# Performance work log

Measured on AMD Instinct MI355X. Metric: run time of the kernel, lower is better.

Reference implementation:

```python
import jax, jax.numpy as jnp
import numpy as np

SEQ_LEN = 2048
EMBED = 1024
HIDDEN = 1024
BATCH = 4


def setup_inputs() -> dict:
    key = jax.random.key(0)
    ks = jax.random.split(key, 7)
    # xavier_uniform for weights: limit = sqrt(6/(fan_in+fan_out))
    lim = float(np.sqrt(6.0 / (EMBED + HIDDEN)))
    blim = float(1.0 / np.sqrt(EMBED))  # torch Linear default bias init U(-1/sqrt(fan_in), ...)
    inputs = jax.random.normal(ks[0], (BATCH, SEQ_LEN, EMBED), dtype=jnp.float32)
    Wq = jax.random.uniform(ks[1], (HIDDEN, EMBED), jnp.float32, -lim, lim)
    Wk = jax.random.uniform(ks[2], (HIDDEN, EMBED), jnp.float32, -lim, lim)
    Wv = jax.random.uniform(ks[3], (HIDDEN, EMBED), jnp.float32, -lim, lim)
    bq = jax.random.uniform(ks[4], (HIDDEN,), jnp.float32, -blim, blim)
    bk = jax.random.uniform(ks[5], (HIDDEN,), jnp.float32, -blim, blim)
    bv = jax.random.uniform(ks[6], (HIDDEN,), jnp.float32, -blim, blim)
    return {"inputs": inputs, "Wq": Wq, "bq": bq, "Wk": Wk, "bk": bk, "Wv": Wv, "bv": bv}


def reference(inputs, Wq, bq, Wk, bk, Wv, bv):
    B, S, E = inputs.shape
    q = jnp.einsum('bse,he->bsh', inputs, Wq) + bq  # [B,S,H]
    k = jnp.einsum('bse,he->bsh', inputs, Wk) + bk
    v = jnp.einsum('bse,he->bsh', inputs, Wv) + bv
    # NOTE: source scales by 1/sqrt(embed_size), not hidden_size
    scores = jnp.einsum('bqh,bkh->bqk', q, k) / jnp.sqrt(jnp.float32(E))
    causal = jnp.tril(jnp.ones((S, S), dtype=bool))  # [S,S]
    scores = jnp.where(causal[None, :, :], scores, -jnp.inf)
    attn = jax.nn.softmax(scores, axis=-1)
    return jnp.einsum('bqk,bkh->bqh', attn, v)
```

## Files before the change

### kernel.cpp

```cpp
#include <hip/hip_runtime.h>
#include <cstdint>
#include <cstddef>
#include <math.h>

typedef unsigned short u16;

#define S_LEN 2048
#define EMB   1024
#define HID   1024
#define NB    4

using bf16x8 = __attribute__((ext_vector_type(8))) __bf16;
using f32x4  = __attribute__((ext_vector_type(4))) float;


__device__ __forceinline__ u16 f2bf(float f) {
  union { float f; uint32_t u; } c; c.f = f;
  uint32_t u = c.u;
  uint32_t r = (u + 0x7fffu + ((u >> 16) & 1u)) >> 16;
  return (u16)r;
}

__device__ __forceinline__ void gld_lds16(const u16* g, u16* l) {
  auto gp = (const __attribute__((address_space(1))) uint32_t*)(uintptr_t)(const void*)g;
  auto lp = (__attribute__((address_space(3))) uint32_t*)(uintptr_t)(void*)l;
  __builtin_amdgcn_global_load_lds(gp, lp, 16, 0, 0);
}


__global__ void cvt_f32_bf16(const float* __restrict__ in, u16* __restrict__ out, int n4) {
  int i = blockIdx.x * blockDim.x + threadIdx.x;
  int stride = gridDim.x * blockDim.x;
  for (; i < n4; i += stride) {
    float4 v = reinterpret_cast<const float4*>(in)[i];
    reinterpret_cast<ushort4*>(out)[i] =
      make_ushort4(f2bf(v.x), f2bf(v.y), f2bf(v.z), f2bf(v.w));
  }
}

__global__ void cvt3_f32_bf16(const float* __restrict__ a, const float* __restrict__ b,
                              const float* __restrict__ c, u16* __restrict__ out, int n4) {
  const float* src = (blockIdx.y == 0) ? a : (blockIdx.y == 1) ? b : c;
  u16* dst = out + (size_t)blockIdx.y * (size_t)n4 * 4;
  int i = blockIdx.x * blockDim.x + threadIdx.x;
  int stride = gridDim.x * blockDim.x;
  for (; i < n4; i += stride) {
    float4 v = reinterpret_cast<const float4*>(src)[i];
    reinterpret_cast<ushort4*>(dst)[i] =
      make_ushort4(f2bf(v.x), f2bf(v.y), f2bf(v.z), f2bf(v.w));
  }
}


template<int EPI>
__global__ __launch_bounds__(512, 2)
void gemm4p(const u16* __restrict__ A, const u16* __restrict__ Bw, void* __restrict__ Cv,
            const float* __restrict__ b0, const float* __restrict__ b1,
            const float* __restrict__ b2, u16* __restrict__ VT,
            int N, int K, long sA, long sB, long sC, float scale)
{
  const int z = blockIdx.z;
  A  += (long)z * sA;
  Bw += (long)z * sB;

  __shared__ __align__(16) u16 smem[49152];

  const int tid = threadIdx.x;
  const int l   = tid & 63;
  const int w   = tid >> 6;
  const int wr  = w >> 2;
  const int wc  = w & 3;

  const int nwg = gridDim.x * gridDim.y;
  const int lin = blockIdx.y * gridDim.x + blockIdx.x;
  const int sw  = (lin & 7) * (nwg >> 3) + (lin >> 3);
  const int bm  = (sw / gridDim.x) * 128;
  const int bn  = (sw % gridDim.x) * 256;

  int kend = K;
  if constexpr (EPI == 3) kend = bm + 128;
  const int NTILE = kend >> 6;

  const int arow = w * 16 + (l >> 2);
  const int acs  = (l & 3) ^ (((l >> 5) & 1) << 1);
  const u16* gbA  = A  + (long)(bm + arow) * K + acs * 8;
  const u16* gbB  = Bw + (long)(bn + arow) * K + acs * 8;
  const u16* gbB2 = gbB + 128L * K;

#define STGH(t, s, dbase)                                                       \
  do {                                                                          \
    const long _o = (long)(t) * 64 + (s) * 32;                                  \
    gld_lds16(gbA  + _o, smem + (dbase) + (s) * 4096 + w * 512);                \
    gld_lds16(gbB  + _o, smem + (dbase) + 8192 + (s) * 8192 + w * 512);         \
    gld_lds16(gbB2 + _o, smem + (dbase) + 8192 + (s) * 8192 + 4096 + w * 512);  \
  } while (0)

  const int lr  = l & 15;
  const int kg  = l >> 4;
  const int kgp = kg ^ (((lr >> 3) & 1) << 1);
  int aoff[4], boff[4];
#pragma unroll
  for (int m = 0; m < 4; ++m) aoff[m] = (wr * 64 + m * 16 + lr) * 32 + kgp * 8;
#pragma unroll
  for (int n = 0; n < 4; ++n) boff[n] = (wc * 64 + n * 16 + lr) * 32 + kgp * 8;

  f32x4 acc[4][4] = {};

  STGH(0, 0, 0);
  STGH(0, 1, 0);
  asm volatile("s_waitcnt vmcnt(0)" ::: "memory");
  __builtin_amdgcn_s_barrier();
  asm volatile("" ::: "memory");

#define PHASE(d, s, STGSTMT)                                                    \
  do {                                                                          \
    const u16* hA = smem + (d) * 24576 + (s) * 4096;                            \
    const u16* hB = smem + (d) * 24576 + 8192 + (s) * 8192;                     \
    bf16x8 av[4], bv[4];                                                        \
    _Pragma("unroll")                                                           \
    for (int m_ = 0; m_ < 4; ++m_)                                              \
      av[m_] = *reinterpret_cast<const bf16x8*>(hA + aoff[m_]);                 \
    _Pragma("unroll")                                                           \
    for (int n_ = 0; n_ < 4; ++n_)                                              \
      bv[n_] = *reinterpret_cast<const bf16x8*>(hB + boff[n_]);                 \
    STGSTMT;                                                                    \
    asm volatile("s_waitcnt vmcnt(3)" ::: "memory");                            \
    __builtin_amdgcn_s_barrier();                                               \
    asm volatile("" ::: "memory");                                              \
    __builtin_amdgcn_s_setprio(1);                                              \
    _Pragma("unroll")                                                           \
    for (int m_ = 0; m_ < 4; ++m_)                                              \
      _Pragma("unroll")                                                         \
      for (int n_ = 0; n_ < 4; ++n_)                                            \
        acc[m_][n_] = __builtin_amdgcn_mfma_f32_16x16x32_bf16(                  \
            av[m_], bv[n_], acc[m_][n_], 0, 0, 0);                              \
    __builtin_amdgcn_s_setprio(0);                                              \
    asm volatile("" ::: "memory");                                              \
  } while (0)

#pragma unroll 1
  for (int i = 0; i < NTILE / 2; ++i) {
    const int t1 = 2 * i + 1;
    const int t2 = (2 * i + 2 < NTILE) ? 2 * i + 2 : NTILE - 1;
    PHASE(0, 0, STGH(t1, 0, 24576));
    PHASE(0, 1, STGH(t1, 1, 24576));
    PHASE(1, 0, STGH(t2, 0, 0));
    PHASE(1, 1, STGH(t2, 1, 0));
  }
#undef PHASE
#undef STGH

  if constexpr (EPI == 3) {
    float* C = (float*)Cv + (long)z * sC;
#pragma unroll
    for (int n = 0; n < 4; ++n) {
      const int col = bn + wc * 64 + n * 16 + lr;
#pragma unroll
      for (int m = 0; m < 4; ++m) {
        const int row0 = bm + wr * 64 + m * 16 + kg * 4;
#pragma unroll
        for (int q = 0; q < 4; ++q)
          C[(long)(row0 + q) * N + col] = acc[m][n][q];
      }
    }
  } else {
    constexpr long M = (long)NB * S_LEN;
    const int sel = bn >> 10;
    const float* bias = (sel == 0) ? b0 : (sel == 1) ? b1 : b2;
    u16* QK = (u16*)Cv;
#pragma unroll
    for (int n = 0; n < 4; ++n) {
      const int col = bn + wc * 64 + n * 16 + lr;
      const int h   = col & (HID - 1);
      const float bbv = bias[h];
#pragma unroll
      for (int m = 0; m < 4; ++m) {
        const int row0 = bm + wr * 64 + m * 16 + kg * 4;
        if (sel < 2) {
          u16* dst = QK + (long)sel * M * HID + (long)row0 * HID + h;
#pragma unroll
          for (int q = 0; q < 4; ++q)
            dst[(long)q * HID] = f2bf(acc[m][n][q] + bbv);
        } else {
          const int b = row0 >> 11;
          const int s = row0 & (S_LEN - 1);
          ushort4 o = make_ushort4(f2bf(acc[m][n][0] + bbv), f2bf(acc[m][n][1] + bbv),
                                   f2bf(acc[m][n][2] + bbv), f2bf(acc[m][n][3] + bbv));
          *reinterpret_cast<ushort4*>(VT + ((long)b * HID + h) * S_LEN + s) = o;
        }
      }
    }
  }
}


__global__ __launch_bounds__(512, 2)
void gemm_pv(const u16* __restrict__ Pm, const u16* __restrict__ VTm, float* __restrict__ Cm)
{
  const int z = blockIdx.z;
  const u16* A = Pm  + (long)z * S_LEN * S_LEN;
  const u16* B = VTm + (long)z * HID * S_LEN;
  float*    Cz = Cm  + (long)z * S_LEN * HID;

  __shared__ __align__(16) u16 smem[32768];

  const int tid = threadIdx.x;
  const int l   = tid & 63;
  const int w   = tid >> 6;
  const int wr  = w >> 2;
  const int wc  = w & 3;
  const int bn  = blockIdx.x * 128;
  const int pr  = blockIdx.y;

  const int lr  = l & 15;
  const int kg  = l >> 4;
  const int kgp = kg ^ (((lr >> 3) & 1) << 1);
  int aoff[4], boff[2];
#pragma unroll
  for (int m = 0; m < 4; ++m) aoff[m] = (wr * 64 + m * 16 + lr) * 32 + kgp * 8;
#pragma unroll
  for (int n = 0; n < 2; ++n) boff[n] = (wc * 32 + n * 16 + lr) * 32 + kgp * 8;

  const int arow = w * 16 + (l >> 2);
  const int acs  = (l & 3) ^ (((l >> 5) & 1) << 1);

#pragma unroll 1
  for (int it = 0; it < 2; ++it) {
    const int bi = (it == 0) ? (15 - pr) : pr;
    const int bm = bi * 128;
    const int NTILE = (bi + 1) * 2;

    const u16* gbA = A + (long)(bm + arow) * S_LEN + acs * 8;
    const u16* gbB = B + (long)(bn + arow) * S_LEN + acs * 8;

#define STGH(t, s, dbase)                                                       \
  do {                                                                          \
    const long _o = (long)(t) * 64 + (s) * 32;                                  \
    gld_lds16(gbA + _o, smem + (dbase) + (s) * 4096 + w * 512);                 \
    gld_lds16(gbB + _o, smem + (dbase) + 8192 + (s) * 4096 + w * 512);          \
  } while (0)

    if (it) {
      __builtin_amdgcn_s_barrier();
      asm volatile("" ::: "memory");
    }

    f32x4 acc[4][2] = {};

    STGH(0, 0, 0);
    STGH(0, 1, 0);
    asm volatile("s_waitcnt vmcnt(0)" ::: "memory");
    __builtin_amdgcn_s_barrier();
    asm volatile("" ::: "memory");

#define PHASE(d, s, STGSTMT)                                                    \
  do {                                                                          \
    const u16* hA = smem + (d) * 16384 + (s) * 4096;                            \
    const u16* hB = smem + (d) * 16384 + 8192 + (s) * 4096;                     \
    bf16x8 av[4], bv[2];                                                        \
    _Pragma("unroll")                                                           \
    for (int m_ = 0; m_ < 4; ++m_)                                              \
      av[m_] = *reinterpret_cast<const bf16x8*>(hA + aoff[m_]);                 \
    _Pragma("unroll")                                                           \
    for (int n_ = 0; n_ < 2; ++n_)                                              \
      bv[n_] = *reinterpret_cast<const bf16x8*>(hB + boff[n_]);                 \
    STGSTMT;                                                                    \
    asm volatile("s_waitcnt vmcnt(2)" ::: "memory");                            \
    __builtin_amdgcn_s_barrier();                                               \
    asm volatile("" ::: "memory");                                              \
    __builtin_amdgcn_s_setprio(1);                                              \
    _Pragma("unroll")                                                           \
    for (int m_ = 0; m_ < 4; ++m_)                                              \
      _Pragma("unroll")                                                         \
      for (int n_ = 0; n_ < 2; ++n_)                                            \
        acc[m_][n_] = __builtin_amdgcn_mfma_f32_16x16x32_bf16(                  \
            av[m_], bv[n_], acc[m_][n_], 0, 0, 0);                              \
    __builtin_amdgcn_s_setprio(0);                                              \
    asm volatile("" ::: "memory");                                              \
  } while (0)

#pragma unroll 1
    for (int i = 0; i < NTILE / 2; ++i) {
      const int t1 = 2 * i + 1;
      const int t2 = (2 * i + 2 < NTILE) ? 2 * i + 2 : NTILE - 1;
      PHASE(0, 0, STGH(t1, 0, 16384));
      PHASE(0, 1, STGH(t1, 1, 16384));
      PHASE(1, 0, STGH(t2, 0, 0));
      PHASE(1, 1, STGH(t2, 1, 0));
    }
#undef PHASE
#undef STGH

#pragma unroll
    for (int n = 0; n < 2; ++n) {
      const int col = bn + wc * 32 + n * 16 + lr;
#pragma unroll
      for (int m = 0; m < 4; ++m) {
        const int row0 = bm + wr * 64 + m * 16 + kg * 4;
#pragma unroll
        for (int q = 0; q < 4; ++q)
          Cz[(long)(row0 + q) * HID + col] = acc[m][n][q];
      }
    }
  }
}


#define BM 128
#define BN 128
#define BK 32

__global__ __launch_bounds__(256)
void gemm_bt2(const u16* __restrict__ A, const u16* __restrict__ B, float* __restrict__ Cv,
              int N, int K, long sA, long sB, long sC, float scale)
{
  const int z = blockIdx.z;
  A += (long)z * sA;
  B += (long)z * sB;

  __shared__ __align__(16) u16 As[BM * BK];
  __shared__ __align__(16) u16 Bs[BN * BK];

  const int t    = threadIdx.x;
  const int lane = t & 63;
  const int wave = t >> 6;
  const int wr   = wave >> 1, wc = wave & 1;

  const int x0 = blockIdx.x;
  const int x  = (x0 & 7) * ((int)gridDim.x >> 3) + (x0 >> 3);
  int bi = (int)((sqrtf(8.0f * (float)x + 1.0f) - 1.0f) * 0.5f);
  while ((bi + 1) * (bi + 2) / 2 <= x) ++bi;
  while (bi * (bi + 1) / 2 > x) --bi;
  const int bm = bi * BM;
  const int bn = (x - bi * (bi + 1) / 2) * BN;

  f32x4 acc[4][4] = {};

  const int r  = t >> 2, c8 = (t & 3) * 8;
  const u16* gA = A + (long)(bm + r) * K + c8;
  const u16* gB = B + (long)(bn + r) * K + c8;
  u16* sA0 = As + wave * 512;
  u16* sB0 = Bs + wave * 512;

  const int lr = lane & 15;
  const int kg = lane >> 4;
  const int aoff = (wr * 64 + lr) * BK + kg * 8;
  const int boff = (wc * 64 + lr) * BK + kg * 8;

  for (int kt = 0; kt < K; kt += BK) {
    gld_lds16(gA,                sA0);
    gld_lds16(gA + 64 * (long)K, sA0 + 2048);
    gld_lds16(gB,                sB0);
    gld_lds16(gB + 64 * (long)K, sB0 + 2048);
    gA += BK; gB += BK;
    __syncthreads();

    bf16x8 af[4], bf[4];
#pragma unroll
    for (int i = 0; i < 4; ++i)
      af[i] = *reinterpret_cast<const bf16x8*>(&As[aoff + i * 16 * BK]);
#pragma unroll
    for (int j = 0; j < 4; ++j)
      bf[j] = *reinterpret_cast<const bf16x8*>(&Bs[boff + j * 16 * BK]);
#pragma unroll
    for (int i = 0; i < 4; ++i)
#pragma unroll
      for (int j = 0; j < 4; ++j)
        acc[i][j] = __builtin_amdgcn_mfma_f32_16x16x32_bf16(af[i], bf[j], acc[i][j], 0, 0, 0);
    __syncthreads();
  }

  float* C = Cv + (long)z * sC;
#pragma unroll
  for (int j = 0; j < 4; ++j) {
    const int col = bn + wc * 64 + j * 16 + lr;
#pragma unroll
    for (int i = 0; i < 4; ++i) {
      const int row0 = bm + wr * 64 + i * 16 + kg * 4;
#pragma unroll
      for (int q = 0; q < 4; ++q) {
        const int row = row0 + q;
        float v = acc[i][j][q] * scale;
        if (col > row) v = -1e30f;
        C[(long)row * N + col] = v;
      }
    }
  }
}


__global__ __launch_bounds__(256)
void softmax_causal(const float* __restrict__ Sc, u16* __restrict__ P, long sS, long sP)
{
  const int row  = blockIdx.x;
  const int z    = blockIdx.y;
  const int kend = ((row >> 7) + 1) << 7;
  const float* srow = Sc + (long)z * sS + (long)row * S_LEN;
  u16*        prow = P  + (long)z * sP + (long)row * S_LEN;
  const int t = threadIdx.x;
  const int lane = t & 63, wave = t >> 6;

  const bool p0 = (4 * t) < kend;
  const bool p1 = (1024 + 4 * t) < kend;

  float4 v0 = make_float4(-1e30f, -1e30f, -1e30f, -1e30f);
  float4 v1 = v0;
  if (p0) v0 = reinterpret_cast<const float4*>(srow)[t];
  if (p1) v1 = reinterpret_cast<const float4*>(srow)[t + 256];

  float mx = fmaxf(fmaxf(fmaxf(v0.x, v0.y), fmaxf(v0.z, v0.w)),
                   fmaxf(fmaxf(v1.x, v1.y), fmaxf(v1.z, v1.w)));

  __shared__ float red[8];
#pragma unroll
  for (int off = 32; off; off >>= 1) mx = fmaxf(mx, __shfl_down(mx, off));
  if (lane == 0) red[wave] = mx;
  __syncthreads();
  mx = fmaxf(fmaxf(red[0], red[1]), fmaxf(red[2], red[3]));

  float e[8];
  e[0] = __expf(v0.x - mx); e[1] = __expf(v0.y - mx);
  e[2] = __expf(v0.z - mx); e[3] = __expf(v0.w - mx);
  e[4] = __expf(v1.x - mx); e[5] = __expf(v1.y - mx);
  e[6] = __expf(v1.z - mx); e[7] = __expf(v1.w - mx);

  float sm = ((e[0] + e[1]) + (e[2] + e[3])) + ((e[4] + e[5]) + (e[6] + e[7]));
#pragma unroll
  for (int off = 32; off; off >>= 1) sm += __shfl_down(sm, off);
  if (lane == 0) red[4 + wave] = sm;
  __syncthreads();
  sm = (red[4] + red[5]) + (red[6] + red[7]);

  const float inv = 1.0f / sm;
  if (p0)
    reinterpret_cast<ushort4*>(prow)[t] =
      make_ushort4(f2bf(e[0]*inv), f2bf(e[1]*inv), f2bf(e[2]*inv), f2bf(e[3]*inv));
  if (p1)
    reinterpret_cast<ushort4*>(prow)[t + 256] =
      make_ushort4(f2bf(e[4]*inv), f2bf(e[5]*inv), f2bf(e[6]*inv), f2bf(e[7]*inv));
}


extern "C" void kernel_launch(void* const* d_in, const int* in_sizes, int n_in,
                              void* d_out, int out_size, void* d_ws, size_t ws_size,
                              hipStream_t stream)
{
  const float* x  = (const float*)d_in[0];
  const float* Wq = (const float*)d_in[1];
  const float* bq = (const float*)d_in[2];
  const float* Wk = (const float*)d_in[3];
  const float* bk = (const float*)d_in[4];
  const float* Wv = (const float*)d_in[5];
  const float* bv = (const float*)d_in[6];
  float* out = (float*)d_out;

  const long M = (long)NB * S_LEN;

  u16* xb  = (u16*)d_ws;
  u16* wqb = xb  + M * EMB;
  u16* Qb  = wqb + 3L * HID * EMB;
  u16* Kb  = Qb  + M * HID;
  u16* VT  = Kb  + M * HID;
  char* rest = (char*)(VT + M * HID);
  const size_t used  = (size_t)(rest - (char*)d_ws);
  const size_t ssz   = (size_t)S_LEN * S_LEN;
  const size_t need4 = used + (size_t)NB * ssz * 4 + (size_t)NB * ssz * 2;
  const int nb = (ws_size >= need4) ? NB : 1;
  float* scores = (float*)rest;
  u16*   P      = (u16*)(rest + (size_t)nb * ssz * 4);

  cvt_f32_bf16<<<2048, 256, 0, stream>>>(x, xb, (int)(M * EMB / 4));
  cvt3_f32_bf16<<<dim3(512, 3), 256, 0, stream>>>(Wq, Wk, Wv, wqb, HID * EMB / 4);

  gemm4p<4><<<dim3(12, 64, 1), 512, 0, stream>>>(xb, wqb, Qb, bq, bk, bv, VT,
                                                 3 * HID, EMB, 0, 0, 0, 1.0f);

  const float scale = 0.03125f;
  const int NTb = S_LEN / BM;
  const int TRI = NTb * (NTb + 1) / 2;

  if (nb == NB) {
    dim3 gs(TRI, 1, NB);
    gemm_bt2<<<gs, 256, 0, stream>>>(Qb, Kb, scores, S_LEN, HID,
                                     (long)S_LEN * HID, (long)S_LEN * HID, (long)ssz, scale);
    softmax_causal<<<dim3(S_LEN, NB), 256, 0, stream>>>(scores, P, (long)ssz, (long)ssz);
    gemm_pv<<<dim3(8, 8, NB), 512, 0, stream>>>(P, VT, out);
  } else {
    for (int b = 0; b < NB; ++b) {
      const u16* Qbb = Qb + (long)b * S_LEN * HID;
      const u16* Kbb = Kb + (long)b * S_LEN * HID;
      const u16* VTb = VT + (long)b * HID * S_LEN;
      float* outb = out + (long)b * S_LEN * HID;
      dim3 gs(TRI, 1, 1);
      gemm_bt2<<<gs, 256, 0, stream>>>(Qbb, Kbb, scores, S_LEN, HID, 0, 0, 0, scale);
      softmax_causal<<<dim3(S_LEN, 1), 256, 0, stream>>>(scores, P, 0, 0);
      gemm_pv<<<dim3(8, 8, 1), 512, 0, stream>>>(P, VTb, outb);
    }
  }
}
```

Baseline: 179.2 us.

## Use pipelined 128x128 gemm template for QK^T scores and shrink QKV tile

Replaces the simple single-buffered gemm_bt2 QK^T kernel with the double-buffered, barrier-pipelined gemm template (now gemmT), generalized to 128x128 tiles with a triangular block mapping and causal masking epilogue. The QKV projection is also switched from 128x256 to 128x128 tiles with twice the grid and K fixed at compile time. This aims to overlap global loads with MFMA work in the scores GEMM and raise occupancy through smaller LDS use, at the cost of lower per-block reuse in the projection GEMM.

```diff
diff --git a/kernel.cpp b/kernel.cpp
--- a/kernel.cpp
+++ b/kernel.cpp
@@ -54,16 +54,18 @@
 
 template<int EPI>
 __global__ __launch_bounds__(512, 2)
-void gemm4p(const u16* __restrict__ A, const u16* __restrict__ Bw, void* __restrict__ Cv,
-            const float* __restrict__ b0, const float* __restrict__ b1,
-            const float* __restrict__ b2, u16* __restrict__ VT,
-            int N, int K, long sA, long sB, long sC, float scale)
+void gemmT(const u16* __restrict__ A, const u16* __restrict__ Bw, void* __restrict__ Cv,
+           const float* __restrict__ b0, const float* __restrict__ b1,
+           const float* __restrict__ b2, u16* __restrict__ VT,
+           int N, long sA, long sB, long sC, float scale)
 {
+  constexpr int K = 1024;
+  constexpr int NTILE = K / 64;
   const int z = blockIdx.z;
   A  += (long)z * sA;
   Bw += (long)z * sB;
 
-  __shared__ __align__(16) u16 smem[49152];
+  __shared__ __align__(16) u16 smem[32768];
 
   const int tid = threadIdx.x;
   const int l   = tid & 63;
@@ -71,40 +73,45 @@
   const int wr  = w >> 2;
   const int wc  = w & 3;
 
-  const int nwg = gridDim.x * gridDim.y;
-  const int lin = blockIdx.y * gridDim.x + blockIdx.x;
-  const int sw  = (lin & 7) * (nwg >> 3) + (lin >> 3);
-  const int bm  = (sw / gridDim.x) * 128;
-  const int bn  = (sw % gridDim.x) * 256;
-
-  int kend = K;
-  if constexpr (EPI == 3) kend = bm + 128;
-  const int NTILE = kend >> 6;
+  int bm, bn;
+  if constexpr (EPI == 2) {
+    const int x0 = blockIdx.x;
+    const int x  = (x0 & 7) * ((int)gridDim.x >> 3) + (x0 >> 3);
+    int bi = (int)((sqrtf(8.0f * (float)x + 1.0f) - 1.0f) * 0.5f);
+    while ((bi + 1) * (bi + 2) / 2 <= x) ++bi;
+    while (bi * (bi + 1) / 2 > x) --bi;
+    bm = bi * 128;
+    bn = (x - bi * (bi + 1) / 2) * 128;
+  } else {
+    const int nwg = gridDim.x * gridDim.y;
+    const int lin = blockIdx.y * gridDim.x + blockIdx.x;
+    const int sw  = (lin & 7) * (nwg >> 3) + (lin >> 3);
+    bm = (sw / gridDim.x) * 128;
+    bn = (sw % gridDim.x) * 128;
+  }
 
   const int arow = w * 16 + (l >> 2);
   const int acs  = (l & 3) ^ (((l >> 5) & 1) << 1);
-  const u16* gbA  = A  + (long)(bm + arow) * K + acs * 8;
-  const u16* gbB  = Bw + (long)(bn + arow) * K + acs * 8;
-  const u16* gbB2 = gbB + 128L * K;
+  const u16* gbA = A  + (long)(bm + arow) * K + acs * 8;
+  const u16* gbB = Bw + (long)(bn + arow) * K + acs * 8;
 
 #define STGH(t, s, dbase)                                                       \
   do {                                                                          \
     const long _o = (long)(t) * 64 + (s) * 32;                                  \
-    gld_lds16(gbA  + _o, smem + (dbase) + (s) * 4096 + w * 512);                \
-    gld_lds16(gbB  + _o, smem + (dbase) + 8192 + (s) * 8192 + w * 512);         \
-    gld_lds16(gbB2 + _o, smem + (dbase) + 8192 + (s) * 8192 + 4096 + w * 512);  \
+    gld_lds16(gbA + _o, smem + (dbase) + (s) * 4096 + w * 512);                 \
+    gld_lds16(gbB + _o, smem + (dbase) + 8192 + (s) * 4096 + w * 512);          \
   } while (0)
 
   const int lr  = l & 15;
   const int kg  = l >> 4;
   const int kgp = kg ^ (((lr >> 3) & 1) << 1);
-  int aoff[4], boff[4];
+  int aoff[4], boff[2];
 #pragma unroll
   for (int m = 0; m < 4; ++m) aoff[m] = (wr * 64 + m * 16 + lr) * 32 + kgp * 8;
 #pragma unroll
-  for (int n = 0; n < 4; ++n) boff[n] = (wc * 64 + n * 16 + lr) * 32 + kgp * 8;
-
-  f32x4 acc[4][4] = {};
+  for (int n = 0; n < 2; ++n) boff[n] = (wc * 32 + n * 16 + lr) * 32 + kgp * 8;
+
+  f32x4 acc[4][2] = {};
 
   STGH(0, 0, 0);
   STGH(0, 1, 0);
@@ -114,24 +121,24 @@
 
 #define PHASE(d, s, STGSTMT)                                                    \
   do {                                                                          \
-    const u16* hA = smem + (d) * 24576 + (s) * 4096;                            \
-    const u16* hB = smem + (d) * 24576 + 8192 + (s) * 8192;                     \
-    bf16x8 av[4], bv[4];                                                        \
+    const u16* hA = smem + (d) * 16384 + (s) * 4096;                            \
+    const u16* hB = smem + (d) * 16384 + 8192 + (s) * 4096;                     \
+    bf16x8 av[4], bv[2];                                                        \
     _Pragma("unroll")                                                           \
     for (int m_ = 0; m_ < 4; ++m_)                                              \
       av[m_] = *reinterpret_cast<const bf16x8*>(hA + aoff[m_]);                 \
     _Pragma("unroll")                                                           \
-    for (int n_ = 0; n_ < 4; ++n_)                                              \
+    for (int n_ = 0; n_ < 2; ++n_)                                              \
       bv[n_] = *reinterpret_cast<const bf16x8*>(hB + boff[n_]);                 \
     STGSTMT;                                                                    \
-    asm volatile("s_waitcnt vmcnt(3)" ::: "memory");                            \
+    asm volatile("s_waitcnt vmcnt(2)" ::: "memory");                            \
     __builtin_amdgcn_s_barrier();                                               \
     asm volatile("" ::: "memory");                                              \
     __builtin_amdgcn_s_setprio(1);                                              \
     _Pragma("unroll")                                                           \
     for (int m_ = 0; m_ < 4; ++m_)                                              \
       _Pragma("unroll")                                                         \
-      for (int n_ = 0; n_ < 4; ++n_)                                            \
+      for (int n_ = 0; n_ < 2; ++n_)                                            \
         acc[m_][n_] = __builtin_amdgcn_mfma_f32_16x16x32_bf16(                  \
             av[m_], bv[n_], acc[m_][n_], 0, 0, 0);                              \
     __builtin_amdgcn_s_setprio(0);                                              \
@@ -142,25 +149,29 @@
   for (int i = 0; i < NTILE / 2; ++i) {
     const int t1 = 2 * i + 1;
     const int t2 = (2 * i + 2 < NTILE) ? 2 * i + 2 : NTILE - 1;
-    PHASE(0, 0, STGH(t1, 0, 24576));
-    PHASE(0, 1, STGH(t1, 1, 24576));
+    PHASE(0, 0, STGH(t1, 0, 16384));
+    PHASE(0, 1, STGH(t1, 1, 16384));
     PHASE(1, 0, STGH(t2, 0, 0));
     PHASE(1, 1, STGH(t2, 1, 0));
   }
 #undef PHASE
 #undef STGH
 
-  if constexpr (EPI == 3) {
+  if constexpr (EPI == 2) {
     float* C = (float*)Cv + (long)z * sC;
 #pragma unroll
-    for (int n = 0; n < 4; ++n) {
-      const int col = bn + wc * 64 + n * 16 + lr;
+    for (int n = 0; n < 2; ++n) {
+      const int col = bn + wc * 32 + n * 16 + lr;
 #pragma unroll
       for (int m = 0; m < 4; ++m) {
         const int row0 = bm + wr * 64 + m * 16 + kg * 4;
 #pragma unroll
-        for (int q = 0; q < 4; ++q)
-          C[(long)(row0 + q) * N + col] = acc[m][n][q];
+        for (int q = 0; q < 4; ++q) {
+          const int row = row0 + q;
+          float v = acc[m][n][q] * scale;
+          if (col > row) v = -1e30f;
+          C[(long)row * N + col] = v;
+        }
       }
     }
   } else {
@@ -169,8 +180,8 @@
     const float* bias = (sel == 0) ? b0 : (sel == 1) ? b1 : b2;
     u16* QK = (u16*)Cv;
 #pragma unroll
-    for (int n = 0; n < 4; ++n) {
-      const int col = bn + wc * 64 + n * 16 + lr;
+    for (int n = 0; n < 2; ++n) {
+      const int col = bn + wc * 32 + n * 16 + lr;
       const int h   = col & (HID - 1);
       const float bbv = bias[h];
 #pragma unroll
@@ -300,89 +311,6 @@
 #pragma unroll
         for (int q = 0; q < 4; ++q)
           Cz[(long)(row0 + q) * HID + col] = acc[m][n][q];
-      }
-    }
-  }
-}
-
-
-#define BM 128
-#define BN 128
-#define BK 32
-
-__global__ __launch_bounds__(256)
-void gemm_bt2(const u16* __restrict__ A, const u16* __restrict__ B, float* __restrict__ Cv,
-              int N, int K, long sA, long sB, long sC, float scale)
-{
-  const int z = blockIdx.z;
-  A += (long)z * sA;
-  B += (long)z * sB;
-
-  __shared__ __align__(16) u16 As[BM * BK];
-  __shared__ __align__(16) u16 Bs[BN * BK];
-
-  const int t    = threadIdx.x;
-  const int lane = t & 63;
-  const int wave = t >> 6;
-  const int wr   = wave >> 1, wc = wave & 1;
-
-  const int x0 = blockIdx.x;
-  const int x  = (x0 & 7) * ((int)gridDim.x >> 3) + (x0 >> 3);
-  int bi = (int)((sqrtf(8.0f * (float)x + 1.0f) - 1.0f) * 0.5f);
-  while ((bi + 1) * (bi + 2) / 2 <= x) ++bi;
-  while (bi * (bi + 1) / 2 > x) --bi;
-  const int bm = bi * BM;
-  const int bn = (x - bi * (bi + 1) / 2) * BN;
-
-  f32x4 acc[4][4] = {};
-
-  const int r  = t >> 2, c8 = (t & 3) * 8;
-  const u16* gA = A + (long)(bm + r) * K + c8;
-  const u16* gB = B + (long)(bn + r) * K + c8;
-  u16* sA0 = As + wave * 512;
-  u16* sB0 = Bs + wave * 512;
-
-  const int lr = lane & 15;
-  const int kg = lane >> 4;
-  const int aoff = (wr * 64 + lr) * BK + kg * 8;
-  const int boff = (wc * 64 + lr) * BK + kg * 8;
-
-  for (int kt = 0; kt < K; kt += BK) {
-    gld_lds16(gA,                sA0);
-    gld_lds16(gA + 64 * (long)K, sA0 + 2048);
-    gld_lds16(gB,                sB0);
-    gld_lds16(gB + 64 * (long)K, sB0 + 2048);
-    gA += BK; gB += BK;
-    __syncthreads();
-
-    bf16x8 af[4], bf[4];
-#pragma unroll
-    for (int i = 0; i < 4; ++i)
-      af[i] = *reinterpret_cast<const bf16x8*>(&As[aoff + i * 16 * BK]);
-#pragma unroll
-    for (int j = 0; j < 4; ++j)
-      bf[j] = *reinterpret_cast<const bf16x8*>(&Bs[boff + j * 16 * BK]);
-#pragma unroll
-    for (int i = 0; i < 4; ++i)
-#pragma unroll
-      for (int j = 0; j < 4; ++j)
-        acc[i][j] = __builtin_amdgcn_mfma_f32_16x16x32_bf16(af[i], bf[j], acc[i][j], 0, 0, 0);
-    __syncthreads();
-  }
-
-  float* C = Cv + (long)z * sC;
-#pragma unroll
-  for (int j = 0; j < 4; ++j) {
-    const int col = bn + wc * 64 + j * 16 + lr;
-#pragma unroll
-    for (int i = 0; i < 4; ++i) {
-      const int row0 = bm + wr * 64 + i * 16 + kg * 4;
-#pragma unroll
-      for (int q = 0; q < 4; ++q) {
-        const int row = row0 + q;
-        float v = acc[i][j][q] * scale;
-        if (col > row) v = -1e30f;
-        C[(long)row * N + col] = v;
       }
     }
   }
@@ -472,17 +400,17 @@
   cvt_f32_bf16<<<2048, 256, 0, stream>>>(x, xb, (int)(M * EMB / 4));
   cvt3_f32_bf16<<<dim3(512, 3), 256, 0, stream>>>(Wq, Wk, Wv, wqb, HID * EMB / 4);
 
-  gemm4p<4><<<dim3(12, 64, 1), 512, 0, stream>>>(xb, wqb, Qb, bq, bk, bv, VT,
-                                                 3 * HID, EMB, 0, 0, 0, 1.0f);
+  gemmT<4><<<dim3(24, 64, 1), 512, 0, stream>>>(xb, wqb, Qb, bq, bk, bv, VT,
+                                                3 * HID, 0, 0, 0, 1.0f);
 
   const float scale = 0.03125f;
-  const int NTb = S_LEN / BM;
-  const int TRI = NTb * (NTb + 1) / 2;
+  const int TRI = 16 * 17 / 2;
 
   if (nb == NB) {
     dim3 gs(TRI, 1, NB);
-    gemm_bt2<<<gs, 256, 0, stream>>>(Qb, Kb, scores, S_LEN, HID,
-                                     (long)S_LEN * HID, (long)S_LEN * HID, (long)ssz, scale);
+    gemmT<2><<<gs, 512, 0, stream>>>(Qb, Kb, scores, nullptr, nullptr, nullptr, nullptr,
+                                     S_LEN, (long)S_LEN * HID, (long)S_LEN * HID,
+                                     (long)ssz, scale);
     softmax_causal<<<dim3(S_LEN, NB), 256, 0, stream>>>(scores, P, (long)ssz, (long)ssz);
     gemm_pv<<<dim3(8, 8, NB), 512, 0, stream>>>(P, VT, out);
   } else {
@@ -492,7 +420,8 @@
       const u16* VTb = VT + (long)b * HID * S_LEN;
       float* outb = out + (long)b * S_LEN * HID;
       dim3 gs(TRI, 1, 1);
-      gemm_bt2<<<gs, 256, 0, stream>>>(Qbb, Kbb, scores, S_LEN, HID, 0, 0, 0, scale);
+      gemmT<2><<<gs, 512, 0, stream>>>(Qbb, Kbb, scores, nullptr, nullptr, nullptr, nullptr,
+                                       S_LEN, 0, 0, 0, scale);
       softmax_causal<<<dim3(S_LEN, 1), 256, 0, stream>>>(scores, P, 0, 0);
       gemm_pv<<<dim3(8, 8, 1), 512, 0, stream>>>(P, VTb, outb);
     }
```

After: 159.7 us. 1.12x faster.
